# Kernel tuning notes

Measured on AMD Instinct MI355X. Metric: run time of the kernel, lower is better.

## Reference

```python
import jax, jax.numpy as jnp
import numpy as np

N = 240000
STRIDE = 4
M = N // STRIDE
C_IN = 32
C_OUT = 64
NSAMPLE = 10  # self.nsample hard-coded to 10 in __init__
MSSC = (1, 2, 4)
K3 = MSSC[2] * NSAMPLE  # 40
EPS = 1e-5


def setup_inputs() -> dict:
    key = jax.random.key(0)
    ks = jax.random.split(key, 10)
    d_in = 3 + C_IN
    s = 1.0 / np.sqrt(d_in)
    s2 = 1.0 / np.sqrt(3 * C_OUT)
    inp = {
        "p": jax.random.normal(ks[0], (N, 3), jnp.float32),
        "x": jax.random.normal(ks[1], (N, C_IN), jnp.float32),
        "o": jnp.array([N], jnp.int32),
        "fps_idx": jax.random.randint(ks[2], (M,), 0, N, dtype=jnp.int32),
        "knn_idx": jax.random.randint(ks[3], (M, K3), 0, N, dtype=jnp.int32),
        "w1": jax.random.uniform(ks[4], (d_in, C_OUT), jnp.float32, -s, s),
        "w2": jax.random.uniform(ks[5], (d_in, C_OUT), jnp.float32, -s, s),
        "w3": jax.random.uniform(ks[6], (d_in, C_OUT), jnp.float32, -s, s),
        "w": jax.random.uniform(ks[7], (3 * C_OUT, C_OUT), jnp.float32, -s2, s2),
        "b": jax.random.uniform(ks[8], (C_OUT,), jnp.float32, -s2, s2),
        "g1": jnp.ones((C_OUT,), jnp.float32),
        "g2": jnp.ones((C_OUT,), jnp.float32),
        "g3": jnp.ones((C_OUT,), jnp.float32),
        "g": jnp.ones((C_OUT,), jnp.float32),
        "be1": jnp.zeros((C_OUT,), jnp.float32),
        "be2": jnp.zeros((C_OUT,), jnp.float32),
        "be3": jnp.zeros((C_OUT,), jnp.float32),
        "be": jnp.zeros((C_OUT,), jnp.float32),
    }
    return inp


def _bn(h, gamma, beta):
    # BatchNorm1d in training mode: per-channel stats over all non-channel axes.
    axes = tuple(range(h.ndim - 1))
    mu = jnp.mean(h, axis=axes, keepdims=True)
    var = jnp.var(h, axis=axes, keepdims=True)
    return (h - mu) * jax.lax.rsqrt(var + EPS) * gamma + beta


def _branch(feat, k, w_s, gamma, beta):
    # linear (no bias) -> BN -> ReLU -> max-pool over k nearest neighbors
    h = jnp.einsum('mkc,co->mko', feat[:, :k], w_s)  # [M,k,O]
    h = jax.nn.relu(_bn(h, gamma, beta))
    return jnp.max(h, axis=1)  # [M,O]


def reference(p, x, o, fps_idx, knn_idx, w1, w2, w3, w, b,
              g1, g2, g3, g, be1, be2, be3, be):
    n_p = p[fps_idx]                                   # [M,3] FPS-sampled centroids
    rel = p[knn_idx] - n_p[:, None, :]                 # [M,K3,3] relative xyz (with_xyz=True)
    feat = jnp.concatenate([rel, x[knn_idx]], axis=-1) # [M,K3,3+C_IN]
    y = jnp.concatenate([
        _branch(feat, MSSC[0] * NSAMPLE, w1, g1, be1),
        _branch(feat, MSSC[1] * NSAMPLE, w2, g2, be2),
        _branch(feat, MSSC[2] * NSAMPLE, w3, g3, be3),
    ], axis=-1)                                        # [M,3*O]
    y = jax.nn.relu(_bn(y @ w + b, g, be))             # [M,O]
    n_o = jnp.array([M], jnp.int32)
    return n_p, y, n_o
```

## Files before the change

### kernel.cpp

```cpp
#include <hip/hip_runtime.h>
#include <hip/hip_bf16.h>

#define K3   40
#define CO   64
#define GM   16
#define CK   20
#define SROW 72
#define FS   200
#define BN_EPS 1e-5f

typedef __attribute__((ext_vector_type(8))) short short8;
typedef __attribute__((ext_vector_type(4))) float f32x4;

static __device__ __forceinline__ short f2bf(float f) {
  union { __hip_bfloat16 b; short s; } u; u.b = __float2bfloat16(f); return u.s;
}
static __device__ __forceinline__ unsigned pk2(float a, float b) {
  union { __hip_bfloat16 b; unsigned short s; } ua, ub;
  ua.b = __float2bfloat16(a); ub.b = __float2bfloat16(b);
  return (unsigned)ua.s | ((unsigned)ub.s << 16);
}


__global__ void k_init(float* __restrict__ stats, float* __restrict__ out_no, int M)
{
  int t = threadIdx.x;
  if (t < 512) stats[t] = 0.f;
  if (t == 0) out_no[0] = (float)M;
}

__global__ void __launch_bounds__(256) k_branch(
    const float* __restrict__ p, const float* __restrict__ x,
    const int* __restrict__ fps, const int* __restrict__ knn,
    const float* __restrict__ w1, const float* __restrict__ w2,
    const float* __restrict__ w3,
    float* __restrict__ hmax1, float* __restrict__ hmax2,
    float* __restrict__ hmax3,
    float* __restrict__ stats, int M)
{
  __shared__ __align__(16) short abuf[CK * GM * SROW];

  const int tid  = threadIdx.x;
  const int wv   = tid >> 6;
  const int lane = tid & 63;
  const int q    = lane >> 4;
  const int nn   = lane & 15;
  const int cg   = wv * 16 + nn;

  short8 bw1[2], bw2[2], bw3[2];
#pragma unroll
  for (int s = 0; s < 2; ++s) {
#pragma unroll
    for (int j = 0; j < 8; ++j) {
      int d = s * 32 + q * 8 + j;
      int row = (d < 32) ? (3 + d) : ((d < 35) ? (d - 32) : -1);
      bw1[s][j] = f2bf(row >= 0 ? w1[row * CO + cg] : 0.f);
      bw2[s][j] = f2bf(row >= 0 ? w2[row * CO + cg] : 0.f);
      bw3[s][j] = f2bf(row >= 0 ? w3[row * CO + cg] : 0.f);
    }
  }

  float s1b0 = 0.f, s1b1 = 0.f, s1b2 = 0.f;
  float s2b0 = 0.f, s2b1 = 0.f, s2b2 = 0.f;

  const int ngrp = M / GM;
  for (int grp = blockIdx.x; grp < ngrp; grp += gridDim.x) {
    const int base = grp * GM;
    float mx1[4], mx2[4], mx3[4];
#pragma unroll
    for (int r = 0; r < 4; ++r) { mx1[r] = -3.4e38f; mx2[r] = -3.4e38f; mx3[r] = -3.4e38f; }

    for (int ch = 0; ch < 2; ++ch) {
      __syncthreads();
      for (int r = tid; r < CK * GM; r += 256) {
        int kl = r >> 4;
        int ml = r & 15;
        int m  = base + ml;
        int k  = ch * CK + kl;
        int gi = knn[m * K3 + k];
        int fi = fps[m];
        const float4* xr = (const float4*)(x + (size_t)gi * 32);
        float4 x0 = xr[0], x1 = xr[1], x2 = xr[2], x3 = xr[3];
        float4 x4 = xr[4], x5 = xr[5], x6 = xr[6], x7 = xr[7];
        float r0 = p[gi * 3 + 0] - p[fi * 3 + 0];
        float r1 = p[gi * 3 + 1] - p[fi * 3 + 1];
        float r2 = p[gi * 3 + 2] - p[fi * 3 + 2];
        uint4 A0 = make_uint4(pk2(x0.x, x0.y), pk2(x0.z, x0.w), pk2(x1.x, x1.y), pk2(x1.z, x1.w));
        uint4 A1 = make_uint4(pk2(x2.x, x2.y), pk2(x2.z, x2.w), pk2(x3.x, x3.y), pk2(x3.z, x3.w));
        uint4 A2 = make_uint4(pk2(x4.x, x4.y), pk2(x4.z, x4.w), pk2(x5.x, x5.y), pk2(x5.z, x5.w));
        uint4 A3 = make_uint4(pk2(x6.x, x6.y), pk2(x6.z, x6.w), pk2(x7.x, x7.y), pk2(x7.z, x7.w));
        uint4 A4 = make_uint4(pk2(r0, r1), pk2(r2, 0.f), 0u, 0u);
        uint4 Z0 = make_uint4(0u, 0u, 0u, 0u);
        uint4* dst = (uint4*)&abuf[r * SROW];
        dst[0] = A0; dst[1] = A1; dst[2] = A2; dst[3] = A3;
        dst[4] = A4; dst[5] = Z0; dst[6] = Z0; dst[7] = Z0;
      }
      __syncthreads();
      for (int kl = 0; kl < CK; ++kl) {
        int kg = ch * CK + kl;
        const short* ar = &abuf[(kl * GM + nn) * SROW + q * 8];
        short8 a0 = *(const short8*)ar;
        short8 a1 = *(const short8*)(ar + 32);
        f32x4 zz = {0.f, 0.f, 0.f, 0.f};
        f32x4 h3 = __builtin_amdgcn_mfma_f32_16x16x32_bf16(a0, bw3[0], zz, 0, 0, 0);
        h3 = __builtin_amdgcn_mfma_f32_16x16x32_bf16(a1, bw3[1], h3, 0, 0, 0);
#pragma unroll
        for (int r = 0; r < 4; ++r) {
          float h = h3[r];
          mx3[r] = fmaxf(mx3[r], h); s1b2 += h; s2b2 = fmaf(h, h, s2b2);
        }
        if (kg < 20) {
          f32x4 h2 = __builtin_amdgcn_mfma_f32_16x16x32_bf16(a0, bw2[0], zz, 0, 0, 0);
          h2 = __builtin_amdgcn_mfma_f32_16x16x32_bf16(a1, bw2[1], h2, 0, 0, 0);
#pragma unroll
          for (int r = 0; r < 4; ++r) {
            float h = h2[r];
            mx2[r] = fmaxf(mx2[r], h); s1b1 += h; s2b1 = fmaf(h, h, s2b1);
          }
          if (kg < 10) {
            f32x4 h1 = __builtin_amdgcn_mfma_f32_16x16x32_bf16(a0, bw1[0], zz, 0, 0, 0);
            h1 = __builtin_amdgcn_mfma_f32_16x16x32_bf16(a1, bw1[1], h1, 0, 0, 0);
#pragma unroll
            for (int r = 0; r < 4; ++r) {
              float h = h1[r];
              mx1[r] = fmaxf(mx1[r], h); s1b0 += h; s2b0 = fmaf(h, h, s2b0);
            }
          }
        }
      }
    }
#pragma unroll
    for (int r = 0; r < 4; ++r) {
      int m = base + q * 4 + r;
      hmax1[(size_t)m * CO + cg] = mx1[r];
      hmax2[(size_t)m * CO + cg] = mx2[r];
      hmax3[(size_t)m * CO + cg] = mx3[r];
    }
  }

  {
    float v;
    v = s1b0; v += __shfl_xor(v, 16); v += __shfl_xor(v, 32);
    if (q == 0) atomicAdd(&stats[0 * 64 + cg], v);
    v = s1b1; v += __shfl_xor(v, 16); v += __shfl_xor(v, 32);
    if (q == 0) atomicAdd(&stats[1 * 64 + cg], v);
    v = s1b2; v += __shfl_xor(v, 16); v += __shfl_xor(v, 32);
    if (q == 0) atomicAdd(&stats[2 * 64 + cg], v);
    v = s2b0; v += __shfl_xor(v, 16); v += __shfl_xor(v, 32);
    if (q == 0) atomicAdd(&stats[192 + 0 * 64 + cg], v);
    v = s2b1; v += __shfl_xor(v, 16); v += __shfl_xor(v, 32);
    if (q == 0) atomicAdd(&stats[192 + 1 * 64 + cg], v);
    v = s2b2; v += __shfl_xor(v, 16); v += __shfl_xor(v, 32);
    if (q == 0) atomicAdd(&stats[192 + 2 * 64 + cg], v);
  }
}

__global__ void k_bn_branch(const float* __restrict__ stats,
                            const float* __restrict__ g1, const float* __restrict__ g2,
                            const float* __restrict__ g3,
                            const float* __restrict__ be1, const float* __restrict__ be2,
                            const float* __restrict__ be3,
                            float* __restrict__ bnp, int M)
{
  int t = threadIdx.x;
  if (t >= 192) return;
  int b = t >> 6, c = t & 63;
  float cnt = (float)M * (float)(10 << b);
  float mu  = stats[t] / cnt;
  float var = stats[192 + t] / cnt - mu * mu;
  const float* g  = (b == 0) ? g1 : ((b == 1) ? g2 : g3);
  const float* be = (b == 0) ? be1 : ((b == 1) ? be2 : be3);
  float sc = g[c] * rsqrtf(var + BN_EPS);
  bnp[t] = sc;
  bnp[192 + t] = be[c] - mu * sc;
}

__global__ void __launch_bounds__(256) k_fuse(
    const float* __restrict__ hmax1, const float* __restrict__ hmax2,
    const float* __restrict__ hmax3,
    const float* __restrict__ bnp, const float* __restrict__ w,
    const float* __restrict__ bias,
    const float* __restrict__ p, const int* __restrict__ fps,
    float* __restrict__ zout, float* __restrict__ stats,
    float* __restrict__ out_np, int M)
{
  __shared__ __align__(16) short ybuf[GM * FS];

  const int tid  = threadIdx.x;
  const int wv   = tid >> 6;
  const int lane = tid & 63;
  const int q    = lane >> 4;
  const int nn   = lane & 15;
  const int cg   = wv * 16 + nn;

  short8 bw[6];
#pragma unroll
  for (int s = 0; s < 6; ++s)
#pragma unroll
    for (int j = 0; j < 8; ++j)
      bw[s][j] = f2bf(w[(s * 32 + q * 8 + j) * CO + cg]);

  const float bia = bias[cg];
  float s1 = 0.f, s2 = 0.f;

  const int ml_s = tid >> 4;
  const int c4   = (tid & 15) * 4;

  const int ngrp = M / GM;
  for (int grp = blockIdx.x; grp < ngrp; grp += gridDim.x) {
    const int base = grp * GM;
#pragma unroll
    for (int b = 0; b < 3; ++b) {
      const float* hb = (b == 0) ? hmax1 : ((b == 1) ? hmax2 : hmax3);
      float4 v  = *(const float4*)&hb[(size_t)(base + ml_s) * CO + c4];
      float4 sc = *(const float4*)&bnp[b * 64 + c4];
      float4 sh = *(const float4*)&bnp[192 + b * 64 + c4];
      float y0 = fmaxf(fmaf(v.x, sc.x, sh.x), 0.f);
      float y1 = fmaxf(fmaf(v.y, sc.y, sh.y), 0.f);
      float y2 = fmaxf(fmaf(v.z, sc.z, sh.z), 0.f);
      float y3 = fmaxf(fmaf(v.w, sc.w, sh.w), 0.f);
      *(uint2*)&ybuf[ml_s * FS + b * 64 + c4] = make_uint2(pk2(y0, y1), pk2(y2, y3));
    }
    if (tid < 48) {
      int ml2 = tid / 3, d = tid - ml2 * 3;
      int fi = fps[base + ml2];
      out_np[(size_t)(base + ml2) * 3 + d] = p[fi * 3 + d];
    }
    __syncthreads();
    const short* ar = &ybuf[nn * FS + q * 8];
    f32x4 acc = {0.f, 0.f, 0.f, 0.f};
#pragma unroll
    for (int s = 0; s < 6; ++s) {
      short8 a = *(const short8*)(ar + s * 32);
      acc = __builtin_amdgcn_mfma_f32_16x16x32_bf16(a, bw[s], acc, 0, 0, 0);
    }
#pragma unroll
    for (int r = 0; r < 4; ++r) {
      float z = acc[r] + bia;
      int m = base + q * 4 + r;
      zout[(size_t)m * CO + cg] = z;
      s1 += z; s2 = fmaf(z, z, s2);
    }
    __syncthreads();
  }

  float v;
  v = s1; v += __shfl_xor(v, 16); v += __shfl_xor(v, 32);
  if (q == 0) atomicAdd(&stats[384 + cg], v);
  v = s2; v += __shfl_xor(v, 16); v += __shfl_xor(v, 32);
  if (q == 0) atomicAdd(&stats[448 + cg], v);
}

__global__ void k_bn_final(const float* __restrict__ stats,
                           const float* __restrict__ g, const float* __restrict__ be,
                           float* __restrict__ bnp, int M)
{
  int c = threadIdx.x;
  if (c >= 64) return;
  float mu  = stats[384 + c] / (float)M;
  float var = stats[448 + c] / (float)M - mu * mu;
  float sc = g[c] * rsqrtf(var + BN_EPS);
  bnp[384 + c] = sc;
  bnp[448 + c] = be[c] - mu * sc;
}

__global__ void k_out(float* __restrict__ y, const float* __restrict__ bnp,
                      float* __restrict__ out_no, int M)
{
  int tid = blockIdx.x * blockDim.x + threadIdx.x;
  int total = M * 64;
  if (tid < total) {
    int c = tid & 63;
    float v = fmaf(y[tid], bnp[384 + c], bnp[448 + c]);
    y[tid] = fmaxf(v, 0.f);
  }
  if (tid == 0) out_no[0] = (float)M;
}

extern "C" void kernel_launch(void* const* d_in, const int* in_sizes, int n_in,
                              void* d_out, int out_size, void* d_ws, size_t ws_size,
                              hipStream_t stream) {
  const float* p   = (const float*)d_in[0];
  const float* x   = (const float*)d_in[1];
  const int*   fps = (const int*)d_in[3];
  const int*   knn = (const int*)d_in[4];
  const float* w1  = (const float*)d_in[5];
  const float* w2  = (const float*)d_in[6];
  const float* w3  = (const float*)d_in[7];
  const float* w   = (const float*)d_in[8];
  const float* b   = (const float*)d_in[9];
  const float* g1  = (const float*)d_in[10];
  const float* g2  = (const float*)d_in[11];
  const float* g3  = (const float*)d_in[12];
  const float* g   = (const float*)d_in[13];
  const float* be1 = (const float*)d_in[14];
  const float* be2 = (const float*)d_in[15];
  const float* be3 = (const float*)d_in[16];
  const float* be  = (const float*)d_in[17];

  const int M = in_sizes[3];

  float* ws    = (float*)d_ws;
  float* hmax1 = ws;
  float* hmax2 = hmax1 + (size_t)M * 64;
  float* hmax3 = hmax2 + (size_t)M * 64;
  float* stats = hmax3 + (size_t)M * 64;
  float* bnp   = stats + 512;

  float* out    = (float*)d_out;
  float* out_np = out;
  float* out_y  = out + (size_t)3 * M;
  float* out_no = out + (size_t)67 * M;

  k_init<<<1, 512, 0, stream>>>(stats, out_no, M);
  k_branch<<<768, 256, 0, stream>>>(p, x, fps, knn, w1, w2, w3,
                                    hmax1, hmax2, hmax3, stats, M);
  k_bn_branch<<<1, 256, 0, stream>>>(stats, g1, g2, g3, be1, be2, be3, bnp, M);
  k_fuse<<<1024, 256, 0, stream>>>(hmax1, hmax2, hmax3, bnp, w, b, p, fps,
                                   out_y, stats, out_np, M);
  k_bn_final<<<1, 64, 0, stream>>>(stats, g, be, bnp, M);
  int total = M * 64;
  k_out<<<(total + 255) / 256, 256, 0, stream>>>(out_y, bnp, out_no, M);
}
```

Measured before the change: 263.4 us.

## Pre-convert x to bf16 and gather MFMA operands directly from global memory

A new pre-pass kernel converts x to bf16 into the output buffer's scratch space, gathers n_p, and zeroes stats. The branch kernel drops the LDS staging of gathered features and instead loads each neighbor's bf16 row straight into MFMA registers, with neighbor indices cached in LDS and the loop split by branch range. The small BN-parameter kernels are folded into k_fuse and k_out, cutting launches from six to four, and grid sizes change. This halves the gathered bytes and removes an LDS round trip and barriers. It adds a full pass over x and relies on per-lane uncoalesced 16-byte gathers.

```diff
diff --git a/kernel.cpp b/kernel.cpp
--- a/kernel.cpp
+++ b/kernel.cpp
@@ -4,8 +4,6 @@
 #define K3   40
 #define CO   64
 #define GM   16
-#define CK   20
-#define SROW 72
 #define FS   200
 #define BN_EPS 1e-5f
 
@@ -22,23 +20,51 @@
 }
 
 
-__global__ void k_init(float* __restrict__ stats, float* __restrict__ out_no, int M)
+__global__ void k_pre(const float* __restrict__ x, const float* __restrict__ p,
+                      const int* __restrict__ fps,
+                      short* __restrict__ xb, float* __restrict__ out_np,
+                      float* __restrict__ stats, float* __restrict__ out_no,
+                      int N, int M)
 {
-  int t = threadIdx.x;
-  if (t < 512) stats[t] = 0.f;
-  if (t == 0) out_no[0] = (float)M;
+  int t = blockIdx.x * blockDim.x + threadIdx.x;
+  int nxb = N * 4;
+  if (t < nxb) {
+    const float4* src = (const float4*)x + (size_t)t * 2;
+    float4 f0 = src[0], f1 = src[1];
+    uint4 o = make_uint4(pk2(f0.x, f0.y), pk2(f0.z, f0.w),
+                         pk2(f1.x, f1.y), pk2(f1.z, f1.w));
+    ((uint4*)xb)[t] = o;
+    return;
+  }
+  int t2 = t - nxb;
+  if (t2 < M) {
+    int fi = fps[t2];
+    float a = p[(size_t)fi * 3 + 0];
+    float b = p[(size_t)fi * 3 + 1];
+    float c = p[(size_t)fi * 3 + 2];
+    out_np[(size_t)t2 * 3 + 0] = a;
+    out_np[(size_t)t2 * 3 + 1] = b;
+    out_np[(size_t)t2 * 3 + 2] = c;
+    return;
+  }
+  int t3 = t2 - M;
+  if (t3 < 512) {
+    stats[t3] = 0.f;
+    if (t3 == 0) out_no[0] = (float)M;
+  }
 }
 
 __global__ void __launch_bounds__(256) k_branch(
-    const float* __restrict__ p, const float* __restrict__ x,
-    const int* __restrict__ fps, const int* __restrict__ knn,
+    const float* __restrict__ p, const short* __restrict__ xb,
+    const float* __restrict__ np, const int* __restrict__ knn,
     const float* __restrict__ w1, const float* __restrict__ w2,
     const float* __restrict__ w3,
     float* __restrict__ hmax1, float* __restrict__ hmax2,
     float* __restrict__ hmax3,
     float* __restrict__ stats, int M)
 {
-  __shared__ __align__(16) short abuf[CK * GM * SROW];
+  __shared__ int   knn_s[GM * 41];
+  __shared__ float np_s[GM * 4];
 
   const int tid  = threadIdx.x;
   const int wv   = tid >> 6;
@@ -62,73 +88,81 @@
 
   float s1b0 = 0.f, s1b1 = 0.f, s1b2 = 0.f;
   float s2b0 = 0.f, s2b1 = 0.f, s2b2 = 0.f;
+  const f32x4 zz = {0.f, 0.f, 0.f, 0.f};
+
+#define LOADA(kg)                                                         \
+    const int gi = knn_s[nn * 41 + (kg)];                                 \
+    const short8 a0 = ((const short8*)(xb + (size_t)gi * 32))[q];         \
+    short8 a1 = {0, 0, 0, 0, 0, 0, 0, 0};                                 \
+    if (q == 0) {                                                         \
+      const float* pg = p + (size_t)gi * 3;                               \
+      a1[0] = f2bf(pg[0] - npx);                                          \
+      a1[1] = f2bf(pg[1] - npy);                                          \
+      a1[2] = f2bf(pg[2] - npz);                                          \
+    }
+
+#define STAT(h, mx, s1, s2)                                               \
+    _Pragma("unroll")                                                     \
+    for (int r = 0; r < 4; ++r) {                                         \
+      float hv = (h)[r];                                                  \
+      (mx)[r] = fmaxf((mx)[r], hv);                                       \
+      (s1) += hv;                                                         \
+      (s2) = fmaf(hv, hv, (s2));                                          \
+    }
 
   const int ngrp = M / GM;
   for (int grp = blockIdx.x; grp < ngrp; grp += gridDim.x) {
     const int base = grp * GM;
+    __syncthreads();
+    for (int i = tid; i < GM * K3; i += 256) {
+      int ml = i / K3, k = i - ml * K3;
+      knn_s[ml * 41 + k] = knn[(size_t)(base + ml) * K3 + k];
+    }
+    if (tid < 48) {
+      int ml = tid / 3, d = tid - ml * 3;
+      np_s[ml * 4 + d] = np[(size_t)(base + ml) * 3 + d];
+    }
+    __syncthreads();
+
+    const float npx = np_s[nn * 4 + 0];
+    const float npy = np_s[nn * 4 + 1];
+    const float npz = np_s[nn * 4 + 2];
+
     float mx1[4], mx2[4], mx3[4];
 #pragma unroll
     for (int r = 0; r < 4; ++r) { mx1[r] = -3.4e38f; mx2[r] = -3.4e38f; mx3[r] = -3.4e38f; }
 
-    for (int ch = 0; ch < 2; ++ch) {
-      __syncthreads();
-      for (int r = tid; r < CK * GM; r += 256) {
-        int kl = r >> 4;
-        int ml = r & 15;
-        int m  = base + ml;
-        int k  = ch * CK + kl;
-        int gi = knn[m * K3 + k];
-        int fi = fps[m];
-        const float4* xr = (const float4*)(x + (size_t)gi * 32);
-        float4 x0 = xr[0], x1 = xr[1], x2 = xr[2], x3 = xr[3];
-        float4 x4 = xr[4], x5 = xr[5], x6 = xr[6], x7 = xr[7];
-        float r0 = p[gi * 3 + 0] - p[fi * 3 + 0];
-        float r1 = p[gi * 3 + 1] - p[fi * 3 + 1];
-        float r2 = p[gi * 3 + 2] - p[fi * 3 + 2];
-        uint4 A0 = make_uint4(pk2(x0.x, x0.y), pk2(x0.z, x0.w), pk2(x1.x, x1.y), pk2(x1.z, x1.w));
-        uint4 A1 = make_uint4(pk2(x2.x, x2.y), pk2(x2.z, x2.w), pk2(x3.x, x3.y), pk2(x3.z, x3.w));
-        uint4 A2 = make_uint4(pk2(x4.x, x4.y), pk2(x4.z, x4.w), pk2(x5.x, x5.y), pk2(x5.z, x5.w));
-        uint4 A3 = make_uint4(pk2(x6.x, x6.y), pk2(x6.z, x6.w), pk2(x7.x, x7.y), pk2(x7.z, x7.w));
-        uint4 A4 = make_uint4(pk2(r0, r1), pk2(r2, 0.f), 0u, 0u);
-        uint4 Z0 = make_uint4(0u, 0u, 0u, 0u);
-        uint4* dst = (uint4*)&abuf[r * SROW];
-        dst[0] = A0; dst[1] = A1; dst[2] = A2; dst[3] = A3;
-        dst[4] = A4; dst[5] = Z0; dst[6] = Z0; dst[7] = Z0;
-      }
-      __syncthreads();
-      for (int kl = 0; kl < CK; ++kl) {
-        int kg = ch * CK + kl;
-        const short* ar = &abuf[(kl * GM + nn) * SROW + q * 8];
-        short8 a0 = *(const short8*)ar;
-        short8 a1 = *(const short8*)(ar + 32);
-        f32x4 zz = {0.f, 0.f, 0.f, 0.f};
-        f32x4 h3 = __builtin_amdgcn_mfma_f32_16x16x32_bf16(a0, bw3[0], zz, 0, 0, 0);
-        h3 = __builtin_amdgcn_mfma_f32_16x16x32_bf16(a1, bw3[1], h3, 0, 0, 0);
-#pragma unroll
-        for (int r = 0; r < 4; ++r) {
-          float h = h3[r];
-          mx3[r] = fmaxf(mx3[r], h); s1b2 += h; s2b2 = fmaf(h, h, s2b2);
-        }
-        if (kg < 20) {
-          f32x4 h2 = __builtin_amdgcn_mfma_f32_16x16x32_bf16(a0, bw2[0], zz, 0, 0, 0);
-          h2 = __builtin_amdgcn_mfma_f32_16x16x32_bf16(a1, bw2[1], h2, 0, 0, 0);
-#pragma unroll
-          for (int r = 0; r < 4; ++r) {
-            float h = h2[r];
-            mx2[r] = fmaxf(mx2[r], h); s1b1 += h; s2b1 = fmaf(h, h, s2b1);
-          }
-          if (kg < 10) {
-            f32x4 h1 = __builtin_amdgcn_mfma_f32_16x16x32_bf16(a0, bw1[0], zz, 0, 0, 0);
-            h1 = __builtin_amdgcn_mfma_f32_16x16x32_bf16(a1, bw1[1], h1, 0, 0, 0);
-#pragma unroll
-            for (int r = 0; r < 4; ++r) {
-              float h = h1[r];
-              mx1[r] = fmaxf(mx1[r], h); s1b0 += h; s2b0 = fmaf(h, h, s2b0);
-            }
-          }
-        }
-      }
-    }
+#pragma unroll 2
+    for (int kg = 0; kg < 10; ++kg) {
+      LOADA(kg)
+      f32x4 h3 = __builtin_amdgcn_mfma_f32_16x16x32_bf16(a0, bw3[0], zz, 0, 0, 0);
+      h3 = __builtin_amdgcn_mfma_f32_16x16x32_bf16(a1, bw3[1], h3, 0, 0, 0);
+      f32x4 h2 = __builtin_amdgcn_mfma_f32_16x16x32_bf16(a0, bw2[0], zz, 0, 0, 0);
+      h2 = __builtin_amdgcn_mfma_f32_16x16x32_bf16(a1, bw2[1], h2, 0, 0, 0);
+      f32x4 h1 = __builtin_amdgcn_mfma_f32_16x16x32_bf16(a0, bw1[0], zz, 0, 0, 0);
+      h1 = __builtin_amdgcn_mfma_f32_16x16x32_bf16(a1, bw1[1], h1, 0, 0, 0);
+      STAT(h3, mx3, s1b2, s2b2)
+      STAT(h2, mx2, s1b1, s2b1)
+      STAT(h1, mx1, s1b0, s2b0)
+    }
+#pragma unroll 2
+    for (int kg = 10; kg < 20; ++kg) {
+      LOADA(kg)
+      f32x4 h3 = __builtin_amdgcn_mfma_f32_16x16x32_bf16(a0, bw3[0], zz, 0, 0, 0);
+      h3 = __builtin_amdgcn_mfma_f32_16x16x32_bf16(a1, bw3[1], h3, 0, 0, 0);
+      f32x4 h2 = __builtin_amdgcn_mfma_f32_16x16x32_bf16(a0, bw2[0], zz, 0, 0, 0);
+      h2 = __builtin_amdgcn_mfma_f32_16x16x32_bf16(a1, bw2[1], h2, 0, 0, 0);
+      STAT(h3, mx3, s1b2, s2b2)
+      STAT(h2, mx2, s1b1, s2b1)
+    }
+#pragma unroll 4
+    for (int kg = 20; kg < 40; ++kg) {
+      LOADA(kg)
+      f32x4 h3 = __builtin_amdgcn_mfma_f32_16x16x32_bf16(a0, bw3[0], zz, 0, 0, 0);
+      h3 = __builtin_amdgcn_mfma_f32_16x16x32_bf16(a1, bw3[1], h3, 0, 0, 0);
+      STAT(h3, mx3, s1b2, s2b2)
+    }
+
 #pragma unroll
     for (int r = 0; r < 4; ++r) {
       int m = base + q * 4 + r;
@@ -137,6 +171,8 @@
       hmax3[(size_t)m * CO + cg] = mx3[r];
     }
   }
+#undef LOADA
+#undef STAT
 
   {
     float v;
@@ -155,36 +191,18 @@
   }
 }
 
-__global__ void k_bn_branch(const float* __restrict__ stats,
-                            const float* __restrict__ g1, const float* __restrict__ g2,
-                            const float* __restrict__ g3,
-                            const float* __restrict__ be1, const float* __restrict__ be2,
-                            const float* __restrict__ be3,
-                            float* __restrict__ bnp, int M)
-{
-  int t = threadIdx.x;
-  if (t >= 192) return;
-  int b = t >> 6, c = t & 63;
-  float cnt = (float)M * (float)(10 << b);
-  float mu  = stats[t] / cnt;
-  float var = stats[192 + t] / cnt - mu * mu;
-  const float* g  = (b == 0) ? g1 : ((b == 1) ? g2 : g3);
-  const float* be = (b == 0) ? be1 : ((b == 1) ? be2 : be3);
-  float sc = g[c] * rsqrtf(var + BN_EPS);
-  bnp[t] = sc;
-  bnp[192 + t] = be[c] - mu * sc;
-}
-
 __global__ void __launch_bounds__(256) k_fuse(
     const float* __restrict__ hmax1, const float* __restrict__ hmax2,
     const float* __restrict__ hmax3,
-    const float* __restrict__ bnp, const float* __restrict__ w,
-    const float* __restrict__ bias,
-    const float* __restrict__ p, const int* __restrict__ fps,
-    float* __restrict__ zout, float* __restrict__ stats,
-    float* __restrict__ out_np, int M)
+    const float* __restrict__ w, const float* __restrict__ bias,
+    const float* __restrict__ g1, const float* __restrict__ g2,
+    const float* __restrict__ g3,
+    const float* __restrict__ be1, const float* __restrict__ be2,
+    const float* __restrict__ be3,
+    float* __restrict__ zout, float* __restrict__ stats, int M)
 {
   __shared__ __align__(16) short ybuf[GM * FS];
+  __shared__ float sc_s[192], sh_s[192];
 
   const int tid  = threadIdx.x;
   const int wv   = tid >> 6;
@@ -193,6 +211,18 @@
   const int nn   = lane & 15;
   const int cg   = wv * 16 + nn;
 
+  if (tid < 192) {
+    int b = tid >> 6, c = tid & 63;
+    float cnt = (float)M * (float)(10 << b);
+    float mu  = stats[tid] / cnt;
+    float var = stats[192 + tid] / cnt - mu * mu;
+    const float* g  = (b == 0) ? g1 : ((b == 1) ? g2 : g3);
+    const float* be = (b == 0) ? be1 : ((b == 1) ? be2 : be3);
+    float sc = g[c] * rsqrtf(var + BN_EPS);
+    sc_s[tid] = sc;
+    sh_s[tid] = be[c] - mu * sc;
+  }
+
   short8 bw[6];
 #pragma unroll
   for (int s = 0; s < 6; ++s)
@@ -205,6 +235,7 @@
 
   const int ml_s = tid >> 4;
   const int c4   = (tid & 15) * 4;
+  __syncthreads();
 
   const int ngrp = M / GM;
   for (int grp = blockIdx.x; grp < ngrp; grp += gridDim.x) {
@@ -213,19 +244,14 @@
     for (int b = 0; b < 3; ++b) {
       const float* hb = (b == 0) ? hmax1 : ((b == 1) ? hmax2 : hmax3);
       float4 v  = *(const float4*)&hb[(size_t)(base + ml_s) * CO + c4];
-      float4 sc = *(const float4*)&bnp[b * 64 + c4];
-      float4 sh = *(const float4*)&bnp[192 + b * 64 + c4];
+      float4 sc = *(const float4*)&sc_s[b * 64 + c4];
+      float4 sh = *(const float4*)&sh_s[b * 64 + c4];
       float y0 = fmaxf(fmaf(v.x, sc.x, sh.x), 0.f);
       float y1 = fmaxf(fmaf(v.y, sc.y, sh.y), 0.f);
       float y2 = fmaxf(fmaf(v.z, sc.z, sh.z), 0.f);
       float y3 = fmaxf(fmaf(v.w, sc.w, sh.w), 0.f);
       *(uint2*)&ybuf[ml_s * FS + b * 64 + c4] = make_uint2(pk2(y0, y1), pk2(y2, y3));
     }
-    if (tid < 48) {
-      int ml2 = tid / 3, d = tid - ml2 * 3;
-      int fi = fps[base + ml2];
-      out_np[(size_t)(base + ml2) * 3 + d] = p[fi * 3 + d];
-    }
     __syncthreads();
     const short* ar = &ybuf[nn * FS + q * 8];
     f32x4 acc = {0.f, 0.f, 0.f, 0.f};
@@ -251,30 +277,33 @@
   if (q == 0) atomicAdd(&stats[448 + cg], v);
 }
 
-__global__ void k_bn_final(const float* __restrict__ stats,
-                           const float* __restrict__ g, const float* __restrict__ be,
-                           float* __restrict__ bnp, int M)
-{
-  int c = threadIdx.x;
-  if (c >= 64) return;
-  float mu  = stats[384 + c] / (float)M;
-  float var = stats[448 + c] / (float)M - mu * mu;
-  float sc = g[c] * rsqrtf(var + BN_EPS);
-  bnp[384 + c] = sc;
-  bnp[448 + c] = be[c] - mu * sc;
-}
-
-__global__ void k_out(float* __restrict__ y, const float* __restrict__ bnp,
+__global__ void k_out(float* __restrict__ y, const float* __restrict__ stats,
+                      const float* __restrict__ g, const float* __restrict__ be,
                       float* __restrict__ out_no, int M)
 {
-  int tid = blockIdx.x * blockDim.x + threadIdx.x;
-  int total = M * 64;
-  if (tid < total) {
-    int c = tid & 63;
-    float v = fmaf(y[tid], bnp[384 + c], bnp[448 + c]);
-    y[tid] = fmaxf(v, 0.f);
-  }
-  if (tid == 0) out_no[0] = (float)M;
+  int t = blockIdx.x * blockDim.x + threadIdx.x;
+  int total = M * 16;
+  if (t < total) {
+    int c0 = (t & 15) * 4;
+    float rm = 1.f / (float)M;
+    float4 v  = ((const float4*)y)[t];
+    float4 sA = *(const float4*)&stats[384 + c0];
+    float4 sB = *(const float4*)&stats[448 + c0];
+    float4 gv = *(const float4*)&g[c0];
+    float4 bv = *(const float4*)&be[c0];
+    float mu0 = sA.x * rm, mu1 = sA.y * rm, mu2 = sA.z * rm, mu3 = sA.w * rm;
+    float sc0 = gv.x * rsqrtf(sB.x * rm - mu0 * mu0 + BN_EPS);
+    float sc1 = gv.y * rsqrtf(sB.y * rm - mu1 * mu1 + BN_EPS);
+    float sc2 = gv.z * rsqrtf(sB.z * rm - mu2 * mu2 + BN_EPS);
+    float sc3 = gv.w * rsqrtf(sB.w * rm - mu3 * mu3 + BN_EPS);
+    float4 o;
+    o.x = fmaxf(fmaf(v.x, sc0, bv.x - mu0 * sc0), 0.f);
+    o.y = fmaxf(fmaf(v.y, sc1, bv.y - mu1 * sc1), 0.f);
+    o.z = fmaxf(fmaf(v.z, sc2, bv.z - mu2 * sc2), 0.f);
+    o.w = fmaxf(fmaf(v.w, sc3, bv.w - mu3 * sc3), 0.f);
+    ((float4*)y)[t] = o;
+  }
+  if (t == 0) out_no[0] = (float)M;
 }
 
 extern "C" void kernel_launch(void* const* d_in, const int* in_sizes, int n_in,
@@ -299,26 +328,27 @@
   const float* be  = (const float*)d_in[17];
 
   const int M = in_sizes[3];
+  const int N = in_sizes[1] / 32;
 
   float* ws    = (float*)d_ws;
   float* hmax1 = ws;
   float* hmax2 = hmax1 + (size_t)M * 64;
   float* hmax3 = hmax2 + (size_t)M * 64;
   float* stats = hmax3 + (size_t)M * 64;
-  float* bnp   = stats + 512;
 
   float* out    = (float*)d_out;
   float* out_np = out;
   float* out_y  = out + (size_t)3 * M;
   float* out_no = out + (size_t)67 * M;
-
-  k_init<<<1, 512, 0, stream>>>(stats, out_no, M);
-  k_branch<<<768, 256, 0, stream>>>(p, x, fps, knn, w1, w2, w3,
-                                    hmax1, hmax2, hmax3, stats, M);
-  k_bn_branch<<<1, 256, 0, stream>>>(stats, g1, g2, g3, be1, be2, be3, bnp, M);
-  k_fuse<<<1024, 256, 0, stream>>>(hmax1, hmax2, hmax3, bnp, w, b, p, fps,
-                                   out_y, stats, out_np, M);
-  k_bn_final<<<1, 64, 0, stream>>>(stats, g, be, bnp, M);
-  int total = M * 64;
-  k_out<<<(total + 255) / 256, 256, 0, stream>>>(out_y, bnp, out_no, M);
-}
+  short* xb     = (short*)out_y;
+
+  int pre_threads = 4 * N + M + 512;
+  k_pre<<<(pre_threads + 255) / 256, 256, 0, stream>>>(x, p, fps, xb, out_np,
+                                                       stats, out_no, N, M);
+  k_branch<<<1250, 256, 0, stream>>>(p, xb, out_np, knn, w1, w2, w3,
+                                     hmax1, hmax2, hmax3, stats, M);
+  k_fuse<<<1250, 256, 0, stream>>>(hmax1, hmax2, hmax3, w, b,
+                                   g1, g2, g3, be1, be2, be3,
+                                   out_y, stats, M);
+  k_out<<<(M * 16 + 255) / 256, 256, 0, stream>>>(out_y, stats, g, be, out_no, M);
+}
```

New measurement: 312.5 us. 18.6% more time.
